# Kernel optimization log

Measured on AMD Instinct MI355X. Metric: run time of the kernel, lower is better.

The kernel has to match this reference:

```python
import jax, jax.numpy as jnp
import numpy as np

# module config (matches init_kwargs)
EMBED = 128; HEADS = 8; HEAD_DIM = EMBED // HEADS  # 16, power of 2
MODES = 16            # hardcoded in FuncSelfAttention
WS = 4                # window_size
SHIFT = 2             # shift_size
NSUB = 8              # n_sub (subdomain grid of the full image)
NW = (NSUB // WS) ** 2   # 4 windows per image
S = WS * WS              # 16 tokens (subdomains) per window
BATCH0 = 4; B = BATCH0 * NW  # 16
P = 32                # per-subdomain spatial resolution (needs P//2+1 >= MODES)
HID = 512             # LogCPB MLP hidden width (Swin-v2 style)


def win_decompose2d(x, nsx, nsy, ws):
    # x: [b, c, H, W] -> [(b*wx*wy), ws*ws, c, sh, sw]
    b, c, H, W = x.shape
    sh = H // nsx; sw = W // nsy
    wx = nsx // ws; wy = nsy // ws
    x = x.reshape(b, c, wx, ws, sh, wy, ws, sw)
    x = x.transpose(0, 2, 5, 3, 6, 1, 4, 7)  # b, wx, wy, qx, qy, c, sh, sw
    return x.reshape(b * wx * wy, ws * ws, c, sh, sw)


def win_recompose2d(x, nsx, nsy, ws):
    # inverse of win_decompose2d: [(b*wx*wy), ws*ws, c, sh, sw] -> [b, c, H, W]
    wx = nsx // ws; wy = nsy // ws
    Bn, s, c, sh, sw = x.shape
    b = Bn // (wx * wy)
    x = x.reshape(b, wx, wy, ws, ws, c, sh, sw)
    x = x.transpose(0, 5, 1, 3, 6, 2, 4, 7)
    return x.reshape(b, c, wx * ws * sh, wy * ws * sw)


def spectral_conv(x, wr, wi):
    # SimpleSpectralConv2d: rfft2 -> low-mode complex channel mixing -> irfft2
    # x: [b, s, cin, h, w]; wr/wi: [cin, cout, m, m]
    m = wr.shape[-1]
    h, w = x.shape[-2:]
    xf = jnp.fft.rfft2(x, axes=(-2, -1))                       # [b,s,cin,h,w//2+1]
    ym = jnp.einsum('bsixy,ioxy->bsoxy', xf[..., :m, :m], wr + 1j * wi)
    out_ft = jnp.zeros(x.shape[:2] + (wr.shape[1], h, w // 2 + 1), dtype=ym.dtype)
    out_ft = out_ft.at[..., :m, :m].set(ym)
    return jnp.fft.irfft2(out_ft, s=(h, w), axes=(-2, -1))


def log_cpb(ws, w1, b1, w2):
    # Swin-v2 style log-spaced continuous position bias MLP -> [heads, S, S]
    g = jnp.arange(ws)
    coords = jnp.stack(jnp.meshgrid(g, g, indexing='ij'), -1).reshape(-1, 2)  # [S,2]
    rel = (coords[:, None, :] - coords[None, :, :]).astype(jnp.float32)       # [S,S,2]
    rel = jnp.sign(rel) * jnp.log2(1.0 + jnp.abs(rel)) / jnp.log2(8.0) * 8.0
    hdn = jax.nn.relu(rel @ w1 + b1)
    return (hdn @ w2).transpose(2, 0, 1)


def _build_attn_mask():
    # Faithful port of the Swin shifted-window mask construction in __init__
    img = np.zeros((NSUB, NSUB), np.float32)
    sl = [slice(0, -WS), slice(-WS, -SHIFT), slice(-SHIFT, None)]
    cnt = 0
    for hs in sl:
        for ws_ in sl:
            img[hs, ws_] = cnt
            cnt += 1
    mw = img.reshape(NSUB // WS, WS, NSUB // WS, WS).transpose(0, 2, 1, 3).reshape(NW, S)
    diff = mw[:, None, :] - mw[:, :, None]
    m = np.where(diff != 0, -1e9, 0.0).astype(np.float32)      # -inf in torch; -1e9 for safe grads
    return np.broadcast_to(m[:, None, :, :], (NW, HEADS, S, S)).copy()


def setup_inputs():
    key = jax.random.key(0)
    ks = jax.random.split(key, 8)
    sc = 1.0 / EMBED
    return {
        'seq': jax.random.normal(ks[0], (B, S, EMBED, P, P), jnp.float32),
        'qkv_wr': jax.random.normal(ks[1], (EMBED, 3 * EMBED, MODES, MODES), jnp.float32) * sc,
        'qkv_wi': jax.random.normal(ks[2], (EMBED, 3 * EMBED, MODES, MODES), jnp.float32) * sc,
        'out_wr': jax.random.normal(ks[3], (EMBED, EMBED, MODES, MODES), jnp.float32) * sc,
        'out_wi': jax.random.normal(ks[4], (EMBED, EMBED, MODES, MODES), jnp.float32) * sc,
        'cpb_w1': jax.random.normal(ks[5], (2, HID), jnp.float32) * 0.1,
        'cpb_b1': jnp.zeros((HID,), jnp.float32),
        'cpb_w2': jax.random.normal(ks[6], (HID, HEADS), jnp.float32) * 0.05,
        'attn_mask': jnp.asarray(_build_attn_mask()),
    }


def reference(seq, qkv_wr, qkv_wi, out_wr, out_wi, cpb_w1, cpb_b1, cpb_w2, attn_mask):
    Bn, s, C, h, w = seq.shape
    ssx = w // WS; ssy = h // WS  # subdomain_size per code: seq.size(-1)//n_sub_x with n_sub_x=window_size
    # shift: recompose windows to images, roll, decompose back
    x = win_recompose2d(seq, WS, WS, WS)
    x = jnp.roll(x, (-SHIFT * ssx, -SHIFT * ssy), axis=(-2, -1))
    x = win_decompose2d(x, WS, WS, WS)
    # qkv = spectral conv + residual tiling (v.repeat with dims[2]=3)
    qkv = spectral_conv(x, qkv_wr, qkv_wi) + jnp.concatenate([x, x, x], axis=2)
    qkv = qkv.reshape(Bn, s, 3, HEADS, HEAD_DIM, h, w)
    q = qkv[:, :, 0].transpose(0, 2, 1, 3, 4, 5)  # [B, H, s, d, h, w]
    k = qkv[:, :, 1].transpose(0, 2, 1, 3, 4, 5)
    v = qkv[:, :, 2].transpose(0, 2, 1, 3, 4, 5)
    bias = attn_mask + log_cpb(WS, cpb_w1, cpb_b1, cpb_w2)[None]  # [nW, H, S, S]
    # 'reimann' scores: Riemann-sum (mean over grid) inner product of q_i, k_j functions
    scale = 1.0 / ((h * w) * jnp.sqrt(jnp.float32(HEAD_DIM)))
    scores = jnp.einsum('bnidxy,bnjdxy->bnij', q, k) * scale      # [B, H, S, S]
    scores = scores.reshape(Bn // NW, NW, HEADS, s, s) + bias[None]
    attn = jax.nn.softmax(scores, axis=-1).reshape(Bn, HEADS, s, s)
    sa = jnp.einsum('bnij,bnjdxy->bnidxy', attn, v)               # [B, H, S, d, h, w]
    sa = sa.transpose(0, 2, 1, 3, 4, 5).reshape(Bn, s, C, h, w)   # _flatten
    sa = spectral_conv(sa, out_wr, out_wi)
    # un-shift
    sa = win_recompose2d(sa, WS, WS, WS)
    sa = jnp.roll(sa, (SHIFT * ssx, SHIFT * ssy), axis=(-2, -1))
    return win_decompose2d(sa, WS, WS, WS)
```

## Files before the change

kernel.cpp:

```cpp
#include <hip/hip_runtime.h>
#include <hip/hip_bf16.h>
#include <math.h>


#define DEVI __device__ __forceinline__
typedef unsigned short u16;
typedef unsigned int u32;
typedef __attribute__((ext_vector_type(8))) short short8;
typedef __attribute__((ext_vector_type(4))) float f32x4;

DEVI u16 f2b(float f) {
  union { __hip_bfloat16 h; u16 u; } cv;
  cv.h = __float2bfloat16(f);
  return cv.u;
}
DEVI float b2f(u16 u) { return __uint_as_float(((u32)u) << 16); }

__global__ __launch_bounds__(256) void k_bias(
    const float* __restrict__ w1, const float* __restrict__ b1,
    const float* __restrict__ w2, const float* __restrict__ amask,
    float* __restrict__ biasb) {
  __shared__ float w1s[1024];
  __shared__ float b1s[512];
  __shared__ float w2s[4096];
  int t = threadIdx.x;
  for (int k = t; k < 1024; k += 256) w1s[k] = w1[k];
  for (int k = t; k < 512; k += 256) b1s[k] = b1[k];
  for (int k = t; k < 4096; k += 256) w2s[k] = w2[k];
  __syncthreads();
  int i = t >> 4, j = t & 15;
  float r0 = (float)((i >> 2) - (j >> 2));
  float r1 = (float)((i & 3) - (j & 3));
  const float sc = 8.0f / 3.0f;
  float f0 = (r0 == 0.f) ? 0.f : copysignf(log2f(1.f + fabsf(r0)) * sc, r0);
  float f1 = (r1 == 0.f) ? 0.f : copysignf(log2f(1.f + fabsf(r1)) * sc, r1);
  float o[8];
#pragma unroll
  for (int h = 0; h < 8; h++) o[h] = 0.f;
  for (int k = 0; k < 512; k++) {
    float hd = f0 * w1s[k] + f1 * w1s[512 + k] + b1s[k];
    hd = fmaxf(hd, 0.f);
#pragma unroll
    for (int h = 0; h < 8; h++) o[h] += hd * w2s[k * 8 + h];
  }
  for (int w = 0; w < 4; w++)
#pragma unroll
    for (int h = 0; h < 8; h++) {
      int idx = ((w * 8 + h) * 16 + i) * 16 + j;
      biasb[idx] = amask[idx] + o[h];
    }
}

__global__ __launch_bounds__(256) void k_transpose_wb(
    const float* __restrict__ wr, const float* __restrict__ wi,
    ushort2* __restrict__ dst, int N) {
  __shared__ ushort2 ld[256][17];
  int t = threadIdx.x;
  int ob = blockIdx.x * 16;
  int cb = blockIdx.y * 8;
  for (int cc = 0; cc < 8; cc++) {
    int c = cb + cc;
    for (int oo = 0; oo < 16; oo++) {
      size_t si = ((size_t)c * N + ob + oo) * 256 + t;
      ushort2 u;
      u.x = f2b(wr[si]);
      u.y = f2b(wi[si]);
      ld[t][oo] = u;
    }
    __syncthreads();
    {
      int oo = t & 15, tq = t >> 4;
#pragma unroll
      for (int mr = 0; mr < 16; mr++) {
        int m = mr * 16 + tq;
        dst[((size_t)m * 128 + c) * N + ob + oo] = ld[m][oo];
      }
    }
    __syncthreads();
  }
}

template <int N>
__global__ __launch_bounds__(256) void k_build_b(
    const ushort2* __restrict__ Ws1, u16* __restrict__ Bt) {
  __shared__ ushort2 tile[128][65];
  int t = threadIdx.x;
  int ob = blockIdx.x;
  int m = blockIdx.y;
  {
    int c4 = t >> 6, o = t & 63;
    for (int cc = 0; cc < 32; cc++) {
      int c = cc * 4 + c4;
      tile[c][o] = Ws1[((size_t)m * 128 + c) * N + ob * 64 + o];
    }
  }
  __syncthreads();
  int l = t & 63, w2 = t >> 6;
  for (int rr = 0; rr < 32; rr++) {
    int r = w2 * 32 + rr;
    int ol = r >> 1, p = r & 1;
    size_t rowoff = ((size_t)m * (2 * N) + (size_t)ob * 128 + r) * 256;
#pragma unroll
    for (int ch = 0; ch < 2; ch++) {
      int c = ch * 64 + l;
      ushort2 wv = tile[c][ol];
      ushort2 u;
      u.x = p ? wv.y : wv.x;
      u.y = p ? wv.x : (u16)(wv.y ^ 0x8000);
      *(ushort2*)(Bt + rowoff + 2 * c) = u;
    }
  }
}

__global__ __launch_bounds__(256) void k_build_wdft(u16* __restrict__ Wdft) {
  int n = blockIdx.x;
  int m = n >> 1, q = n & 1;
  int kx = m >> 4, ky = m & 15;
  int t = threadIdx.x;
#pragma unroll
  for (int i = 0; i < 4; i++) {
    int p = i * 256 + t;
    int u = p >> 5, v = p & 31;
    int ph = (kx * u + ky * v) & 31;
    float th = 6.283185307179586f * (float)ph / 32.f;
    float sv, cv;
    sincosf(th, &sv, &cv);
    Wdft[(size_t)n * 1024 + p] = f2b(q ? -sv : cv);
  }
}

__global__ __launch_bounds__(256) void k_build_widft(u16* __restrict__ Widf) {
  int p = blockIdx.x;
  int x = p >> 5, y = p & 31;
  for (int n = threadIdx.x; n < 512; n += 256) {
    int m = n >> 1, q = n & 1;
    int kx = m >> 4, ky = m & 15;
    int ph = (kx * x + ky * y) & 31;
    float th = 6.283185307179586f * (float)ph / 32.f;
    float sv, cv;
    sincosf(th, &sv, &cv);
    float cky = (ky == 0) ? (1.f / 1024.f) : (2.f / 1024.f);
    Widf[(size_t)p * 512 + n] = f2b(q ? -sv * cky : cv * cky);
  }
}

__global__ __launch_bounds__(256) void k_gather(
    const float* __restrict__ seq, u16* __restrict__ Tbf) {
  int t = threadIdx.x;
  int cq = blockIdx.x;
  int bs = blockIdx.y;
  int b = bs >> 4, s = bs & 15;
  int qx = s >> 2, qy = s & 3;
  int u = t >> 3, vb = (t & 7) * 4;
  int uu = u + 16;
  int u2 = uu & 31;
  int qx2 = (qx + (uu >> 5)) & 3;
  int vv = vb + 16;
  int v2 = vv & 31;
  int qy2 = (qy + (vv >> 5)) & 3;
  int s2 = qx2 * 4 + qy2;
  size_t srcbase = (((size_t)(b * 16 + s2) * 128) << 10) + u2 * 32 + v2;
  size_t dstbase = (((size_t)bs * 128) << 10) + u * 32 + vb;
  for (int cc = 0; cc < 32; cc++) {
    size_t coff = (size_t)(cq * 32 + cc) << 10;
    float4 v = *(const float4*)(seq + srcbase + coff);
    ushort4 o;
    o.x = f2b(v.x);
    o.y = f2b(v.y);
    o.z = f2b(v.z);
    o.w = f2b(v.w);
    *(ushort4*)(Tbf + dstbase + coff) = o;
  }
}

__global__ __launch_bounds__(512) void k_dftm(
    const u16* __restrict__ Wdft, const u16* __restrict__ Tbf,
    u16* __restrict__ Xbf) {
  __shared__ char lds[49152];
  char* As = lds;
  char* Bs = lds + 32768;
  u16* st = (u16*)lds;
  int t = threadIdx.x;
  int mt = blockIdx.x, bs = blockIdx.y;
  int l = t & 63, w = t >> 6;
  int wm = w >> 1, wn = w & 1;
  f32x4 acc[4][4];
#pragma unroll
  for (int a_ = 0; a_ < 4; a_++)
#pragma unroll
    for (int b_ = 0; b_ < 4; b_++) acc[a_][b_] = (f32x4){0.f, 0.f, 0.f, 0.f};
  const u16* Ab = Wdft + (size_t)mt * 256 * 1024;
  const u16* Bb = Tbf + (size_t)bs * 128 * 1024;
  int srow = t >> 3, ss = t & 7;
  uint4 ra[4], rb[2];
#pragma unroll
  for (int i = 0; i < 4; i++)
    ra[i] = *(const uint4*)(Ab + (size_t)(i * 64 + srow) * 1024 + ss * 8);
#pragma unroll
  for (int i = 0; i < 2; i++)
    rb[i] = *(const uint4*)(Bb + (size_t)(i * 64 + srow) * 1024 + ss * 8);
  for (int kt = 0; kt < 16; kt++) {
    if (kt) __syncthreads();
#pragma unroll
    for (int i = 0; i < 4; i++) {
      int row = i * 64 + srow;
      *(uint4*)(As + row * 128 + ((ss ^ (row & 7)) << 4)) = ra[i];
    }
#pragma unroll
    for (int i = 0; i < 2; i++) {
      int row = i * 64 + srow;
      *(uint4*)(Bs + row * 128 + ((ss ^ (row & 7)) << 4)) = rb[i];
    }
    if (kt < 15) {
#pragma unroll
      for (int i = 0; i < 4; i++)
        ra[i] = *(const uint4*)(Ab + (size_t)(i * 64 + srow) * 1024 +
                                (kt + 1) * 64 + ss * 8);
#pragma unroll
      for (int i = 0; i < 2; i++)
        rb[i] = *(const uint4*)(Bb + (size_t)(i * 64 + srow) * 1024 +
                                (kt + 1) * 64 + ss * 8);
    }
    __syncthreads();
#pragma unroll
    for (int kk = 0; kk < 2; kk++) {
      short8 af[4], bg[4];
#pragma unroll
      for (int fm = 0; fm < 4; fm++) {
        int row = wm * 64 + fm * 16 + (l & 15);
        int chunk = kk * 4 + (l >> 4);
        af[fm] = *(const short8*)(As + row * 128 + ((chunk ^ (row & 7)) << 4));
      }
#pragma unroll
      for (int fn = 0; fn < 4; fn++) {
        int row = wn * 64 + fn * 16 + (l & 15);
        int chunk = kk * 4 + (l >> 4);
        bg[fn] = *(const short8*)(Bs + row * 128 + ((chunk ^ (row & 7)) << 4));
      }
#pragma unroll
      for (int fm = 0; fm < 4; fm++)
#pragma unroll
        for (int fn = 0; fn < 4; fn++)
          acc[fm][fn] = __builtin_amdgcn_mfma_f32_16x16x32_bf16(
              af[fm], bg[fn], acc[fm][fn], 0, 0, 0);
    }
  }
  int cr = (l >> 4) * 4, ccol = l & 15;
  for (int pass = 0; pass < 2; pass++) {
    __syncthreads();
    if ((wm >> 1) == pass) {
#pragma unroll
      for (int fm = 0; fm < 4; fm++) {
#pragma unroll
        for (int fn = 0; fn < 4; fn++) {
          int c = wn * 64 + fn * 16 + ccol;
#pragma unroll
          for (int rp = 0; rp < 4; rp += 2) {
            int rloc = (wm & 1) * 32 + fm * 8 + ((cr + rp) >> 1);
            ushort2 ub;
            ub.x = f2b(acc[fm][fn][rp]);
            ub.y = f2b(acc[fm][fn][rp + 1]);
            *(ushort2*)(st + rloc * 264 + 2 * c) = ub;
          }
        }
      }
    }
    __syncthreads();
#pragma unroll
    for (int it = 0; it < 4; it++) {
      int idx = it * 512 + t;
      int row = idx >> 5;
      int ch = idx & 31;
      uint4 v = *(const uint4*)(st + row * 264 + ch * 8);
      int m = mt * 128 + pass * 64 + row;
      *(uint4*)(Xbf + ((size_t)bs * 256 + m) * 256 + ch * 8) = v;
    }
  }
}

__global__ __launch_bounds__(64) void k_gram_mfma(
    const u16* __restrict__ Tbf, float* __restrict__ Gpart) {
  int dc = blockIdx.x;
  int bh = blockIdx.y;
  int b = bh >> 3, h = bh & 7;
  int l = threadIdx.x;
  f32x4 a0 = (f32x4){0.f, 0.f, 0.f, 0.f};
  f32x4 a1 = (f32x4){0.f, 0.f, 0.f, 0.f};
  const u16* base =
      Tbf + ((size_t)(b * 16 + (l & 15)) * 128 + h * 16 + dc * 4) * 1024;
  int ko = (l >> 4) * 8;
  for (int kk = 0; kk < 128; kk += 2) {
    short8 f0 = *(const short8*)(base + kk * 32 + ko);
    short8 f1 = *(const short8*)(base + kk * 32 + 32 + ko);
    a0 = __builtin_amdgcn_mfma_f32_16x16x32_bf16(f0, f0, a0, 0, 0, 0);
    a1 = __builtin_amdgcn_mfma_f32_16x16x32_bf16(f1, f1, a1, 0, 0, 0);
  }
  float* dst = Gpart + ((size_t)(dc * 16 + b) * 8 + h) * 256;
#pragma unroll
  for (int r = 0; r < 4; r++)
    dst[((l >> 4) * 4 + r) * 16 + (l & 15)] = a0[r] + a1[r];
}

template <int NP>
__global__ __launch_bounds__(512) void k_mixm(
    const u16* __restrict__ A, const u16* __restrict__ Bm,
    u16* __restrict__ Cb) {
  __shared__ char lds[65536];
  char* As = lds;
  char* Bs = lds + 32768;
  u16* st = (u16*)lds;
  int t = threadIdx.x;
  const int gx = NP / 256;
  int orig = blockIdx.y * gx + blockIdx.x;
  const int tot = gx * 256;
  int lid = (orig & 7) * (tot >> 3) + (orig >> 3);
  int nt = lid % gx;
  int m = lid / gx;
  int l = t & 63, w = t >> 6;
  int wm = w >> 1, wn = w & 1;
  f32x4 acc[4][8];
#pragma unroll
  for (int a_ = 0; a_ < 4; a_++)
#pragma unroll
    for (int b_ = 0; b_ < 8; b_++) acc[a_][b_] = (f32x4){0.f, 0.f, 0.f, 0.f};
  const u16* Bb = Bm + ((size_t)m * NP + nt * 256) * 256;
  int srow = t >> 3, ss = t & 7;
  uint4 ra[4], rb[4];
#pragma unroll
  for (int i = 0; i < 4; i++) {
    int row = i * 64 + srow;
    ra[i] = *(const uint4*)(A + ((size_t)row * 256 + m) * 256 + ss * 8);
    rb[i] = *(const uint4*)(Bb + (size_t)row * 256 + ss * 8);
  }
  for (int kt = 0; kt < 4; kt++) {
    if (kt) __syncthreads();
#pragma unroll
    for (int i = 0; i < 4; i++) {
      int row = i * 64 + srow;
      int sw = ((ss ^ (row & 7)) << 4);
      *(uint4*)(As + row * 128 + sw) = ra[i];
      *(uint4*)(Bs + row * 128 + sw) = rb[i];
    }
    if (kt < 3) {
#pragma unroll
      for (int i = 0; i < 4; i++) {
        int row = i * 64 + srow;
        ra[i] = *(const uint4*)(A + ((size_t)row * 256 + m) * 256 +
                                (kt + 1) * 64 + ss * 8);
        rb[i] =
            *(const uint4*)(Bb + (size_t)row * 256 + (kt + 1) * 64 + ss * 8);
      }
    }
    __syncthreads();
#pragma unroll
    for (int kk = 0; kk < 2; kk++) {
      short8 af[4], bg[8];
#pragma unroll
      for (int fm = 0; fm < 4; fm++) {
        int row = wm * 64 + fm * 16 + (l & 15);
        int chunk = kk * 4 + (l >> 4);
        af[fm] = *(const short8*)(As + row * 128 + ((chunk ^ (row & 7)) << 4));
      }
#pragma unroll
      for (int fn = 0; fn < 8; fn++) {
        int row = wn * 128 + fn * 16 + (l & 15);
        int chunk = kk * 4 + (l >> 4);
        bg[fn] = *(const short8*)(Bs + row * 128 + ((chunk ^ (row & 7)) << 4));
      }
#pragma unroll
      for (int fm = 0; fm < 4; fm++)
#pragma unroll
        for (int fn = 0; fn < 8; fn++)
          acc[fm][fn] = __builtin_amdgcn_mfma_f32_16x16x32_bf16(
              bg[fn], af[fm], acc[fm][fn], 0, 0, 0);
    }
  }
#pragma unroll
  for (int fm = 0; fm < 4; fm++) {
    __syncthreads();
    int rloc = wm * 16 + (l & 15);
#pragma unroll
    for (int fn = 0; fn < 8; fn++) {
      int col = wn * 128 + fn * 16 + (l >> 4) * 4;
      ushort4 u;
      u.x = f2b(acc[fm][fn][0]);
      u.y = f2b(acc[fm][fn][1]);
      u.z = f2b(acc[fm][fn][2]);
      u.w = f2b(acc[fm][fn][3]);
      *(ushort4*)(st + rloc * 264 + col) = u;
    }
    __syncthreads();
#pragma unroll
    for (int it = 0; it < 4; it++) {
      int idx = it * 512 + t;
      int row = idx >> 5;
      int ch = idx & 31;
      uint4 v = *(const uint4*)(st + row * 264 + ch * 8);
      int bs = (row >> 4) * 64 + fm * 16 + (row & 15);
      *(uint4*)(Cb + ((size_t)nt * 65536 + (size_t)m * 256 + bs) * 256 +
                ch * 8) = v;
    }
  }
}

__global__ __launch_bounds__(256) void k_transp_out(
    const ushort2* __restrict__ OUTb2, ushort2* __restrict__ OUTt2) {
  __shared__ ushort2 ld[128][129];
  int t = threadIdx.x;
  int bs = blockIdx.x;
  for (int mh = 0; mh < 2; mh++) {
    if (mh) __syncthreads();
    {
      int cidx = t & 127;
      int rb = t >> 7;
      for (int pass = 0; pass < 64; pass++) {
        int r = pass * 2 + rb;
        ld[r][cidx] = OUTb2[((size_t)(mh * 128 + r) * 256 + bs) * 128 + cidx];
      }
    }
    __syncthreads();
    {
      int ml = t & 127;
      int cb = t >> 7;
      for (int pass = 0; pass < 64; pass++) {
        int c = pass * 2 + cb;
        OUTt2[((size_t)bs * 128 + c) * 256 + mh * 128 + ml] = ld[ml][c];
      }
    }
  }
}

__global__ __launch_bounds__(512) void k_irfftm(
    const u16* __restrict__ Widf, const u16* __restrict__ OUTt,
    u16* __restrict__ tmp) {
  __shared__ char lds[49152];
  char* As = lds;
  char* Bs = lds + 32768;
  u16* st = (u16*)lds;
  int t = threadIdx.x;
  int ph = blockIdx.x, bs = blockIdx.y;
  int l = t & 63, w = t >> 6;
  int wm = w >> 1, wn = w & 1;
  f32x4 acc[4][4];
#pragma unroll
  for (int a_ = 0; a_ < 4; a_++)
#pragma unroll
    for (int b_ = 0; b_ < 4; b_++) acc[a_][b_] = (f32x4){0.f, 0.f, 0.f, 0.f};
  const u16* Ab = Widf + (size_t)ph * 256 * 512;
  const u16* Bb = OUTt + (size_t)bs * 128 * 512;
  int srow = t >> 3, ss = t & 7;
  uint4 ra[4], rb[2];
#pragma unroll
  for (int i = 0; i < 4; i++)
    ra[i] = *(const uint4*)(Ab + (size_t)(i * 64 + srow) * 512 + ss * 8);
#pragma unroll
  for (int i = 0; i < 2; i++)
    rb[i] = *(const uint4*)(Bb + (size_t)(i * 64 + srow) * 512 + ss * 8);
  for (int kt = 0; kt < 8; kt++) {
    if (kt) __syncthreads();
#pragma unroll
    for (int i = 0; i < 4; i++) {
      int row = i * 64 + srow;
      *(uint4*)(As + row * 128 + ((ss ^ (row & 7)) << 4)) = ra[i];
    }
#pragma unroll
    for (int i = 0; i < 2; i++) {
      int row = i * 64 + srow;
      *(uint4*)(Bs + row * 128 + ((ss ^ (row & 7)) << 4)) = rb[i];
    }
    if (kt < 7) {
#pragma unroll
      for (int i = 0; i < 4; i++)
        ra[i] = *(const uint4*)(Ab + (size_t)(i * 64 + srow) * 512 +
                                (kt + 1) * 64 + ss * 8);
#pragma unroll
      for (int i = 0; i < 2; i++)
        rb[i] = *(const uint4*)(Bb + (size_t)(i * 64 + srow) * 512 +
                                (kt + 1) * 64 + ss * 8);
    }
    __syncthreads();
#pragma unroll
    for (int kk = 0; kk < 2; kk++) {
      short8 wf[4], bg[4];
#pragma unroll
      for (int fm = 0; fm < 4; fm++) {
        int row = wm * 64 + fm * 16 + (l & 15);
        int chunk = kk * 4 + (l >> 4);
        wf[fm] = *(const short8*)(As + row * 128 + ((chunk ^ (row & 7)) << 4));
      }
#pragma unroll
      for (int fn = 0; fn < 4; fn++) {
        int row = wn * 64 + fn * 16 + (l & 15);
        int chunk = kk * 4 + (l >> 4);
        bg[fn] = *(const short8*)(Bs + row * 128 + ((chunk ^ (row & 7)) << 4));
      }
#pragma unroll
      for (int fm = 0; fm < 4; fm++)
#pragma unroll
        for (int fn = 0; fn < 4; fn++)
          acc[fm][fn] = __builtin_amdgcn_mfma_f32_16x16x32_bf16(
              wf[fm], bg[fn], acc[fm][fn], 0, 0, 0);
    }
  }
  for (int pass = 0; pass < 2; pass++) {
    __syncthreads();
    if ((wm >> 1) == pass) {
#pragma unroll
      for (int fm = 0; fm < 4; fm++)
#pragma unroll
        for (int fn = 0; fn < 4; fn++) {
          int c = wn * 64 + fn * 16 + (l & 15);
#pragma unroll
          for (int r = 0; r < 4; r++) {
            int pl = (wm & 1) * 64 + fm * 16 + (l >> 4) * 4 + r;
            st[pl * 136 + c] = f2b(acc[fm][fn][r]);
          }
        }
    }
    __syncthreads();
#pragma unroll
    for (int it = 0; it < 4; it++) {
      int idx = it * 512 + t;
      int row = idx >> 4;
      int ch = idx & 15;
      uint4 v = *(const uint4*)(st + row * 136 + ch * 8);
      int p = ph * 256 + pass * 128 + row;
      *(uint4*)(tmp + ((size_t)bs * 1024 + p) * 128 + ch * 8) = v;
    }
  }
}

__global__ __launch_bounds__(256) void k_unshift(
    const u16* __restrict__ tmp, float* __restrict__ out) {
  __shared__ float ld[2][32][33];
  int t = threadIdx.x;
  int cq = blockIdx.x;
  int bs2 = blockIdx.y;
  int b = bs2 >> 4, s2 = bs2 & 15;
  int qx2 = s2 >> 2, qy2 = s2 & 3;
  int r = t >> 3;
  int y = (r < 16) ? r + 16 : r - 16;
  int qy = (r < 16) ? (qy2 + 3) & 3 : qy2;
  int cl4 = (t & 7) * 4;
  int cs = t >> 3;
  int vh = (t & 7) * 4;
  for (int u2 = 0; u2 < 32; u2++) {
    int cu = u2 & 1;
    int x = (u2 < 16) ? u2 + 16 : u2 - 16;
    int qx = (u2 < 16) ? (qx2 + 3) & 3 : qx2;
    {
      int bs_src = b * 16 + qx * 4 + qy;
      const u16* src =
          tmp + ((size_t)bs_src * 1024 + x * 32 + y) * 128 + cq * 32;
      ushort4 v = *(const ushort4*)(src + cl4);
      ld[cu][r][cl4 + 0] = b2f(v.x);
      ld[cu][r][cl4 + 1] = b2f(v.y);
      ld[cu][r][cl4 + 2] = b2f(v.z);
      ld[cu][r][cl4 + 3] = b2f(v.w);
    }
    __syncthreads();
    {
      float* dst =
          out + (((size_t)bs2 * 128 + cq * 32 + cs) << 10) + u2 * 32 + vh;
      float4 v = make_float4(ld[cu][vh + 0][cs], ld[cu][vh + 1][cs],
                             ld[cu][vh + 2][cs], ld[cu][vh + 3][cs]);
      *(float4*)dst = v;
    }
  }
}

__global__ __launch_bounds__(256) void k_scores(
    const ushort2* __restrict__ Xb2, const ushort2* __restrict__ Qb2,
    const ushort2* __restrict__ Kb2, float* __restrict__ Spart) {
  __shared__ float2 Xs[16][17], Qs[16][17], Ks[16][17];
  int t = threadIdx.x;
  int mc = blockIdx.x;
  int bh = blockIdx.y;
  int b = bh >> 3, h = bh & 7;
  int i = t >> 4, j = t & 15;
  int bs = b * 16 + i;
  int d = j;
  int m0 = mc * 32;
  size_t xoff = ((size_t)bs * 256 + m0) * 128 + h * 16 + d;
  size_t qoff = ((size_t)m0 * 256 + bs) * 128 + h * 16 + d;
  ushort2 ux = Xb2[xoff];
  ushort2 uq = Qb2[qoff];
  ushort2 uk = Kb2[qoff];
  float acc = 0.f;
  for (int mm = 0; mm < 32; mm++) {
    int m = m0 + mm;
    Xs[i][d] = make_float2(b2f(ux.x), b2f(ux.y));
    Qs[i][d] = make_float2(b2f(uq.x), b2f(uq.y));
    Ks[i][d] = make_float2(b2f(uk.x), b2f(uk.y));
    __syncthreads();
    if (mm < 31) {
      ux = Xb2[xoff + (size_t)(mm + 1) * 128];
      uq = Qb2[qoff + (size_t)(mm + 1) * 32768];
      uk = Kb2[qoff + (size_t)(mm + 1) * 32768];
    }
    int ky = m & 15, kx = m >> 4;
    if (ky > 0) {
#pragma unroll
      for (int dd = 0; dd < 16; dd++) {
        float2 Xi = Xs[i][dd], Qi = Qs[i][dd], Xj = Xs[j][dd], Kj = Ks[j][dd];
        float qr = Xi.x + Qi.x, qi = Xi.y + Qi.y;
        float kr = Xj.x + Kj.x, ki = Xj.y + Kj.y;
        acc += 2.f * (qr * kr + qi * ki - (Xi.x * Xj.x + Xi.y * Xj.y));
      }
    } else {
#pragma unroll
      for (int dd = 0; dd < 16; dd++) {
        float2 Xi = Xs[i][dd], Qi = Qs[i][dd], Xj = Xs[j][dd], Kj = Ks[j][dd];
        float cr = Xi.x * Kj.x + Xi.y * Kj.y + Qi.x * Xj.x + Qi.y * Xj.y;
        float qk =
            (kx == 0) ? (Qi.x * Kj.x) : 0.5f * (Qi.x * Kj.x + Qi.y * Kj.y);
        acc += cr + qk;
      }
    }
    __syncthreads();
  }
  Spart[((size_t)mc * 128 + bh) * 256 + t] = acc;
}

__global__ __launch_bounds__(256) void k_softmax(
    const float* __restrict__ Spart, const float* __restrict__ Gpart,
    const float* __restrict__ biasb, float* __restrict__ attn) {
  int t = threadIdx.x;
  int bh = blockIdx.x;
  int b = bh >> 3, h = bh & 7;
  int i = t >> 4, j = t & 15;
  float acc = 0.f;
#pragma unroll
  for (int mc = 0; mc < 8; mc++)
    acc += Spart[((size_t)mc * 128 + bh) * 256 + t];
  float G = 0.f;
#pragma unroll
  for (int dc = 0; dc < 4; dc++)
    G += Gpart[((size_t)(dc * 16 + b) * 8 + h) * 256 + t];
  float score = G * (1.f / 4096.f) + acc * (1.f / 4194304.f) +
                biasb[(((b & 3) * 8 + h) * 16 + i) * 16 + j];
  float mx = score;
#pragma unroll
  for (int o = 8; o >= 1; o >>= 1) mx = fmaxf(mx, __shfl_xor(mx, o, 16));
  float e = expf(score - mx);
  float sm = e;
#pragma unroll
  for (int o = 8; o >= 1; o >>= 1) sm += __shfl_xor(sm, o, 16);
  attn[(size_t)bh * 256 + t] = e / sm;
}

__global__ __launch_bounds__(256) void k_sav(
    const ushort2* __restrict__ Xb2, const ushort2* __restrict__ Vb2,
    const float* __restrict__ attn, ushort2* __restrict__ SAfb) {
  __shared__ float at[8][16][17];
  __shared__ float2 vt[16][130];
  int t = threadIdx.x;
  int mc = blockIdx.x;
  int b = blockIdx.y;
  {
    int h = t >> 5, ii = (t >> 1) & 15, jb = (t & 1) * 8;
#pragma unroll
    for (int k = 0; k < 8; k++)
      at[h][ii][jb + k] = attn[((size_t)(b * 8 + h) * 16 + ii) * 16 + jb + k];
  }
  __syncthreads();
  int i = t >> 4, cg = t & 15;
  for (int mm = 0; mm < 16; mm++) {
    int m = mc * 16 + mm;
    int ky = m & 15, kx = m >> 4;
    {
      int jj = t >> 4;
      size_t vrow = ((size_t)m * 256 + b * 16 + jj) * 128;
      size_t xrow = ((size_t)(b * 16 + jj) * 256 + m) * 128;
#pragma unroll
      for (int u = 0; u < 8; u++) {
        int c = cg + u * 16;
        ushort2 uv = Vb2[vrow + c];
        float2 vm = make_float2(b2f(uv.x), b2f(uv.y));
        ushort2 uxv = Xb2[xrow + c];
        float2 xv = make_float2(b2f(uxv.x), b2f(uxv.y));
        float2 vh;
        if (ky == 0) {
          if (kx == 0)
            vh = make_float2(xv.x + vm.x, xv.y);
          else
            vh = make_float2(xv.x + 0.5f * vm.x, xv.y + 0.5f * vm.y);
        } else
          vh = make_float2(xv.x + vm.x, xv.y + vm.y);
        vt[jj][c] = vh;
      }
    }
    __syncthreads();
    float2 o8[8];
#pragma unroll
    for (int u = 0; u < 8; u++) o8[u] = make_float2(0.f, 0.f);
#pragma unroll
    for (int jj = 0; jj < 16; jj++) {
#pragma unroll
      for (int u = 0; u < 8; u++) {
        float av = at[u][i][jj];
        float2 v = vt[jj][cg + u * 16];
        o8[u].x += av * v.x;
        o8[u].y += av * v.y;
      }
    }
    size_t orow = ((size_t)(b * 16 + i) * 256 + m) * 128;
#pragma unroll
    for (int u = 0; u < 8; u++) {
      ushort2 ub;
      ub.x = f2b(o8[u].x);
      ub.y = f2b(o8[u].y);
      SAfb[orow + cg + u * 16] = ub;
    }
    __syncthreads();
  }
}

extern "C" void kernel_launch(void* const* d_in, const int* in_sizes, int n_in,
                              void* d_out, int out_size, void* d_ws,
                              size_t ws_size, hipStream_t stream) {
  (void)in_sizes;
  (void)n_in;
  const float* seq = (const float*)d_in[0];
  const float* qwr = (const float*)d_in[1];
  const float* qwi = (const float*)d_in[2];
  const float* owr = (const float*)d_in[3];
  const float* owi = (const float*)d_in[4];
  const float* cw1 = (const float*)d_in[5];
  const float* cb1 = (const float*)d_in[6];
  const float* cw2 = (const float*)d_in[7];
  const float* amask = (const float*)d_in[8];
  float* out = (float*)d_out;
  char* ws = (char*)d_ws;

  const size_t R = 100663296;
  ushort2* Wq_s1b = (ushort2*)ws;
  u16* Tbf = (u16*)ws;
  u16* Xbf = (u16*)(ws + 67108864);
  ushort2* Xb2 = (ushort2*)Xbf;
  u16* Wob = (u16*)ws;
  u16* QKV = (u16*)(ws + R);
  ushort2* Qb2 = (ushort2*)QKV;
  ushort2* Kb2 = Qb2 + 8388608;
  ushort2* Vb2 = Qb2 + 16777216;
  u16* OUTb = (u16*)(ws + R);
  u16* OUTt = (u16*)(ws + R + 33554432);
  u16* tmpb = (u16*)(ws + R + 2 * 33554432);
  u16* Wqb = (u16*)(ws + 2 * R);
  ushort2* SAfb = (ushort2*)(ws + 2 * R);
  ushort2* Wo_s1b = (ushort2*)(ws + 3 * R);
  char* sm = ws + 3 * R + 16777216 + 67108864;
  u16* Wdft = (u16*)sm;
  float* Gpart = (float*)(sm + 1048576);
  float* biasb = (float*)(sm + 1572864);
  float* attn = (float*)(sm + 1605632);
  float* Spart = (float*)(sm + 1736704);
  u16* Widf = (u16*)(sm + 2785280);
  size_t need = 3 * R + 16777216 + 67108864 + 2785280 + 1048576;

  if (ws_size < need) {
    hipMemsetAsync(d_out, 0, (size_t)out_size * 4, stream);
    return;
  }

  dim3 blk(256);
  k_transpose_wb<<<dim3(24, 16), blk, 0, stream>>>(qwr, qwi, Wq_s1b, 384);
  k_build_b<384><<<dim3(6, 256), blk, 0, stream>>>(Wq_s1b, Wqb);
  k_transpose_wb<<<dim3(8, 16), blk, 0, stream>>>(owr, owi, Wo_s1b, 128);
  k_bias<<<dim3(1), blk, 0, stream>>>(cw1, cb1, cw2, amask, biasb);
  k_build_wdft<<<dim3(512), blk, 0, stream>>>(Wdft);
  k_build_widft<<<dim3(1024), blk, 0, stream>>>(Widf);
  k_gather<<<dim3(4, 256), blk, 0, stream>>>(seq, Tbf);
  k_dftm<<<dim3(2, 256), dim3(512), 0, stream>>>(Wdft, Tbf, Xbf);
  k_gram_mfma<<<dim3(4, 128), dim3(64), 0, stream>>>(Tbf, Gpart);
  k_mixm<768><<<dim3(3, 256), dim3(512), 0, stream>>>(Xbf, Wqb, QKV);
  k_scores<<<dim3(8, 128), blk, 0, stream>>>(Xb2, Qb2, Kb2, Spart);
  k_softmax<<<dim3(128), blk, 0, stream>>>(Spart, Gpart, biasb, attn);
  k_build_b<128><<<dim3(2, 256), blk, 0, stream>>>(Wo_s1b, Wob);
  k_sav<<<dim3(16, 16), blk, 0, stream>>>(Xb2, Vb2, attn, SAfb);
  k_mixm<256><<<dim3(1, 256), dim3(512), 0, stream>>>((const u16*)SAfb, Wob,
                                                      OUTb);
  k_transp_out<<<dim3(256), blk, 0, stream>>>((const ushort2*)OUTb,
                                              (ushort2*)OUTt);
  k_irfftm<<<dim3(4, 256), dim3(512), 0, stream>>>(Widf, OUTt, tmpb);
  k_unshift<<<dim3(4, 256), blk, 0, stream>>>(tmpb, out);
}
```

Measured before the change: 818.6 us.

## Fuse shifted gather and bf16 conversion into DFT GEMM and Gram kernels

Removes the separate gather kernel that rolled the input and wrote a bf16 copy. The DFT GEMM now loads the rolled fp32 input directly and packs it to bf16 while staging into shared memory. The Gram kernel also reads the fp32 input directly and reduces its four channel chunks inside the block, so softmax reads a single Gram buffer. This saves one launch and a full write plus re-read of the intermediate tensor. In exchange the input is read twice in fp32, with narrower 32-byte row segments that may coalesce less well.

```diff
diff --git a/kernel.cpp b/kernel.cpp
--- a/kernel.cpp
+++ b/kernel.cpp
@@ -15,6 +15,9 @@
   return cv.u;
 }
 DEVI float b2f(u16 u) { return __uint_as_float(((u32)u) << 16); }
+DEVI u32 pk2(float a, float b) {
+  return (u32)f2b(a) | ((u32)f2b(b) << 16);
+}
 
 __global__ __launch_bounds__(256) void k_bias(
     const float* __restrict__ w1, const float* __restrict__ b1,
@@ -144,37 +147,8 @@
   }
 }
 
-__global__ __launch_bounds__(256) void k_gather(
-    const float* __restrict__ seq, u16* __restrict__ Tbf) {
-  int t = threadIdx.x;
-  int cq = blockIdx.x;
-  int bs = blockIdx.y;
-  int b = bs >> 4, s = bs & 15;
-  int qx = s >> 2, qy = s & 3;
-  int u = t >> 3, vb = (t & 7) * 4;
-  int uu = u + 16;
-  int u2 = uu & 31;
-  int qx2 = (qx + (uu >> 5)) & 3;
-  int vv = vb + 16;
-  int v2 = vv & 31;
-  int qy2 = (qy + (vv >> 5)) & 3;
-  int s2 = qx2 * 4 + qy2;
-  size_t srcbase = (((size_t)(b * 16 + s2) * 128) << 10) + u2 * 32 + v2;
-  size_t dstbase = (((size_t)bs * 128) << 10) + u * 32 + vb;
-  for (int cc = 0; cc < 32; cc++) {
-    size_t coff = (size_t)(cq * 32 + cc) << 10;
-    float4 v = *(const float4*)(seq + srcbase + coff);
-    ushort4 o;
-    o.x = f2b(v.x);
-    o.y = f2b(v.y);
-    o.z = f2b(v.z);
-    o.w = f2b(v.w);
-    *(ushort4*)(Tbf + dstbase + coff) = o;
-  }
-}
-
 __global__ __launch_bounds__(512) void k_dftm(
-    const u16* __restrict__ Wdft, const u16* __restrict__ Tbf,
+    const u16* __restrict__ Wdft, const float* __restrict__ seq,
     u16* __restrict__ Xbf) {
   __shared__ char lds[49152];
   char* As = lds;
@@ -182,6 +156,8 @@
   u16* st = (u16*)lds;
   int t = threadIdx.x;
   int mt = blockIdx.x, bs = blockIdx.y;
+  int b = bs >> 4, s = bs & 15;
+  int qx = s >> 2, qy = s & 3;
   int l = t & 63, w = t >> 6;
   int wm = w >> 1, wn = w & 1;
   f32x4 acc[4][4];
@@ -190,15 +166,29 @@
 #pragma unroll
     for (int b_ = 0; b_ < 4; b_++) acc[a_][b_] = (f32x4){0.f, 0.f, 0.f, 0.f};
   const u16* Ab = Wdft + (size_t)mt * 256 * 1024;
-  const u16* Bb = Tbf + (size_t)bs * 128 * 1024;
   int srow = t >> 3, ss = t & 7;
-  uint4 ra[4], rb[2];
+  int vband = (ss & 3) * 8;
+  int vv = vband + 16;
+  int v2 = vv & 31;
+  int qy2 = (qy + (vv >> 5)) & 3;
+  uint4 ra[4];
+  float4 rf[2][2];
 #pragma unroll
   for (int i = 0; i < 4; i++)
     ra[i] = *(const uint4*)(Ab + (size_t)(i * 64 + srow) * 1024 + ss * 8);
 #pragma unroll
-  for (int i = 0; i < 2; i++)
-    rb[i] = *(const uint4*)(Bb + (size_t)(i * 64 + srow) * 1024 + ss * 8);
+  for (int i = 0; i < 2; i++) {
+    int c = i * 64 + srow;
+    int u = (ss >> 2);
+    int uu = u + 16;
+    int u2 = uu & 31;
+    int qx2 = (qx + (uu >> 5)) & 3;
+    const float* src = seq +
+                       (((size_t)(b * 16 + qx2 * 4 + qy2) * 128 + c) << 10) +
+                       u2 * 32 + v2;
+    rf[i][0] = *(const float4*)src;
+    rf[i][1] = *(const float4*)(src + 4);
+  }
   for (int kt = 0; kt < 16; kt++) {
     if (kt) __syncthreads();
 #pragma unroll
@@ -209,17 +199,31 @@
 #pragma unroll
     for (int i = 0; i < 2; i++) {
       int row = i * 64 + srow;
-      *(uint4*)(Bs + row * 128 + ((ss ^ (row & 7)) << 4)) = rb[i];
+      uint4 bv;
+      bv.x = pk2(rf[i][0].x, rf[i][0].y);
+      bv.y = pk2(rf[i][0].z, rf[i][0].w);
+      bv.z = pk2(rf[i][1].x, rf[i][1].y);
+      bv.w = pk2(rf[i][1].z, rf[i][1].w);
+      *(uint4*)(Bs + row * 128 + ((ss ^ (row & 7)) << 4)) = bv;
     }
     if (kt < 15) {
 #pragma unroll
       for (int i = 0; i < 4; i++)
         ra[i] = *(const uint4*)(Ab + (size_t)(i * 64 + srow) * 1024 +
                                 (kt + 1) * 64 + ss * 8);
-#pragma unroll
-      for (int i = 0; i < 2; i++)
-        rb[i] = *(const uint4*)(Bb + (size_t)(i * 64 + srow) * 1024 +
-                                (kt + 1) * 64 + ss * 8);
+      int u = (kt + 1) * 2 + (ss >> 2);
+      int uu = u + 16;
+      int u2 = uu & 31;
+      int qx2 = (qx + (uu >> 5)) & 3;
+      size_t base = (((size_t)(b * 16 + qx2 * 4 + qy2) * 128) << 10) +
+                    u2 * 32 + v2;
+#pragma unroll
+      for (int i = 0; i < 2; i++) {
+        int c = i * 64 + srow;
+        const float* src = seq + base + ((size_t)c << 10);
+        rf[i][0] = *(const float4*)src;
+        rf[i][1] = *(const float4*)(src + 4);
+      }
     }
     __syncthreads();
 #pragma unroll
@@ -278,27 +282,53 @@
   }
 }
 
-__global__ __launch_bounds__(64) void k_gram_mfma(
-    const u16* __restrict__ Tbf, float* __restrict__ Gpart) {
-  int dc = blockIdx.x;
-  int bh = blockIdx.y;
+__global__ __launch_bounds__(256) void k_gram_seq(
+    const float* __restrict__ seq, float* __restrict__ Gfull) {
+  __shared__ float red[3][256];
+  int t = threadIdx.x;
+  int bh = blockIdx.x;
   int b = bh >> 3, h = bh & 7;
-  int l = threadIdx.x;
-  f32x4 a0 = (f32x4){0.f, 0.f, 0.f, 0.f};
-  f32x4 a1 = (f32x4){0.f, 0.f, 0.f, 0.f};
-  const u16* base =
-      Tbf + ((size_t)(b * 16 + (l & 15)) * 128 + h * 16 + dc * 4) * 1024;
+  int w = t >> 6, l = t & 63;
+  int tok = l & 15;
+  int qx = tok >> 2, qy = tok & 3;
   int ko = (l >> 4) * 8;
-  for (int kk = 0; kk < 128; kk += 2) {
-    short8 f0 = *(const short8*)(base + kk * 32 + ko);
-    short8 f1 = *(const short8*)(base + kk * 32 + 32 + ko);
-    a0 = __builtin_amdgcn_mfma_f32_16x16x32_bf16(f0, f0, a0, 0, 0, 0);
-    a1 = __builtin_amdgcn_mfma_f32_16x16x32_bf16(f1, f1, a1, 0, 0, 0);
-  }
-  float* dst = Gpart + ((size_t)(dc * 16 + b) * 8 + h) * 256;
-#pragma unroll
-  for (int r = 0; r < 4; r++)
-    dst[((l >> 4) * 4 + r) * 16 + (l & 15)] = a0[r] + a1[r];
+  int v2 = (ko < 16) ? ko + 16 : ko - 16;
+  int qy2 = (ko < 16) ? qy : (qy + 1) & 3;
+  f32x4 a = (f32x4){0.f, 0.f, 0.f, 0.f};
+  for (int cc = 0; cc < 4; cc++) {
+    int c = h * 16 + w * 4 + cc;
+#pragma unroll 4
+    for (int u = 0; u < 32; u++) {
+      int uu = u + 16;
+      int u2 = uu & 31;
+      int qx2 = (qx + (uu >> 5)) & 3;
+      const float* src = seq +
+                         (((size_t)(b * 16 + qx2 * 4 + qy2) * 128 + c) << 10) +
+                         u2 * 32 + v2;
+      float4 lo = *(const float4*)src;
+      float4 hi = *(const float4*)(src + 4);
+      union { short8 s8; uint4 u4; } f;
+      f.u4.x = pk2(lo.x, lo.y);
+      f.u4.y = pk2(lo.z, lo.w);
+      f.u4.z = pk2(hi.x, hi.y);
+      f.u4.w = pk2(hi.z, hi.w);
+      a = __builtin_amdgcn_mfma_f32_16x16x32_bf16(f.s8, f.s8, a, 0, 0, 0);
+    }
+  }
+  if (w > 0) {
+#pragma unroll
+    for (int r = 0; r < 4; r++)
+      red[w - 1][((l >> 4) * 4 + r) * 16 + (l & 15)] = a[r];
+  }
+  __syncthreads();
+  if (w == 0) {
+#pragma unroll
+    for (int r = 0; r < 4; r++) {
+      int idx = ((l >> 4) * 4 + r) * 16 + (l & 15);
+      Gfull[(size_t)bh * 256 + idx] =
+          a[r] + red[0][idx] + red[1][idx] + red[2][idx];
+    }
+  }
 }
 
 template <int NP>
@@ -623,7 +653,7 @@
 }
 
 __global__ __launch_bounds__(256) void k_softmax(
-    const float* __restrict__ Spart, const float* __restrict__ Gpart,
+    const float* __restrict__ Spart, const float* __restrict__ Gfull,
     const float* __restrict__ biasb, float* __restrict__ attn) {
   int t = threadIdx.x;
   int bh = blockIdx.x;
@@ -633,10 +663,7 @@
 #pragma unroll
   for (int mc = 0; mc < 8; mc++)
     acc += Spart[((size_t)mc * 128 + bh) * 256 + t];
-  float G = 0.f;
-#pragma unroll
-  for (int dc = 0; dc < 4; dc++)
-    G += Gpart[((size_t)(dc * 16 + b) * 8 + h) * 256 + t];
+  float G = Gfull[(size_t)bh * 256 + t];
   float score = G * (1.f / 4096.f) + acc * (1.f / 4194304.f) +
                 biasb[(((b & 3) * 8 + h) * 16 + i) * 16 + j];
   float mx = score;
@@ -735,7 +762,6 @@
 
   const size_t R = 100663296;
   ushort2* Wq_s1b = (ushort2*)ws;
-  u16* Tbf = (u16*)ws;
   u16* Xbf = (u16*)(ws + 67108864);
   ushort2* Xb2 = (ushort2*)Xbf;
   u16* Wob = (u16*)ws;
@@ -751,7 +777,7 @@
   ushort2* Wo_s1b = (ushort2*)(ws + 3 * R);
   char* sm = ws + 3 * R + 16777216 + 67108864;
   u16* Wdft = (u16*)sm;
-  float* Gpart = (float*)(sm + 1048576);
+  float* Gfull = (float*)(sm + 1048576);
   float* biasb = (float*)(sm + 1572864);
   float* attn = (float*)(sm + 1605632);
   float* Spart = (float*)(sm + 1736704);
@@ -770,12 +796,11 @@
   k_bias<<<dim3(1), blk, 0, stream>>>(cw1, cb1, cw2, amask, biasb);
   k_build_wdft<<<dim3(512), blk, 0, stream>>>(Wdft);
   k_build_widft<<<dim3(1024), blk, 0, stream>>>(Widf);
-  k_gather<<<dim3(4, 256), blk, 0, stream>>>(seq, Tbf);
-  k_dftm<<<dim3(2, 256), dim3(512), 0, stream>>>(Wdft, Tbf, Xbf);
-  k_gram_mfma<<<dim3(4, 128), dim3(64), 0, stream>>>(Tbf, Gpart);
+  k_dftm<<<dim3(2, 256), dim3(512), 0, stream>>>(Wdft, seq, Xbf);
+  k_gram_seq<<<dim3(128), blk, 0, stream>>>(seq, Gfull);
   k_mixm<768><<<dim3(3, 256), dim3(512), 0, stream>>>(Xbf, Wqb, QKV);
   k_scores<<<dim3(8, 128), blk, 0, stream>>>(Xb2, Qb2, Kb2, Spart);
-  k_softmax<<<dim3(128), blk, 0, stream>>>(Spart, Gpart, biasb, attn);
+  k_softmax<<<dim3(128), blk, 0, stream>>>(Spart, Gfull, biasb, attn);
   k_build_b<128><<<dim3(2, 256), blk, 0, stream>>>(Wo_s1b, Wob);
   k_sav<<<dim3(16, 16), blk, 0, stream>>>(Xb2, Vb2, attn, SAfb);
   k_mixm<256><<<dim3(1, 256), dim3(512), 0, stream>>>((const u16*)SAfb, Wob,
```

New measurement: 792.4 us. -3.2%, faster.
